# Kernel optimization log

Hardware: AMD Instinct MI355X
Metric: run time of the kernel (lower is better)

## Reference

```python
import jax, jax.numpy as jnp
import numpy as np

N, D, A, NQ, G1, G2 = 2048, 512, 64, 8, 8, 8
A1 = 2 * A  # tier-1 MQA uses att_dim*2 internally


def setup_inputs() -> dict:
    key = jax.random.key(0)
    ks = iter(jax.random.split(key, 24))
    r = lambda *sh: (jax.random.normal(next(ks), sh, dtype=jnp.float32) * 0.02)
    return {
        "x": jax.random.normal(next(ks), (N, D), dtype=jnp.float32),
        # tier 1 (num_groups_first MQA blocks, inner dim A1)
        "Wq1": r(G1, NQ, D, A1), "bq1": r(G1, NQ, A1),
        "Wk1": r(G1, D, A1),     "bk1": r(G1, A1),
        "Wv1": r(G1, D, A1),     "bv1": r(G1, A1),
        "Wo1": r(G1, NQ * A1, D), "bo1": r(G1, D),
        # tier 2 (num_groups_second MQA blocks, inner dim A)
        "Wq2": r(G2, NQ, D, A), "bq2": r(G2, NQ, A),
        "Wk2": r(G2, D, A),     "bk2": r(G2, A),
        "Wv2": r(G2, D, A),     "bv2": r(G2, A),
        "Wo2": r(G2, NQ * A, D), "bo2": r(G2, D),
        # final projection: in = att_dim * num_groups_second == D
        "Wo": r(D, D), "bo": r(D),
    }


def _mqa_grouped(xg, Wq, bq, Wk, bk, Wv, bv, Wo, bo):
    """Batched MultiQueryAttention over a group axis g.
    xg: [g, n, d]; Wq: [g, q, d, a]. No softmax (per source)."""
    a = Wq.shape[-1]
    q = jnp.einsum('gnd,gqda->gqna', xg, Wq) + bq[:, :, None, :]
    k = jnp.einsum('gnd,gda->gna', xg, Wk) + bk[:, None, :]
    v = jnp.einsum('gnd,gda->gna', xg, Wv) + bv[:, None, :]
    scores = jnp.einsum('gqna,gma->gqnm', q, k) / jnp.sqrt(jnp.asarray(a, jnp.float32))
    ctx = jnp.einsum('gqnm,gma->gqna', scores, v)          # [g,q,n,a]
    g, nq, n, ad = ctx.shape
    ctx = ctx.transpose(0, 2, 1, 3).reshape(g, n, nq * ad)  # concat queries on feat dim
    return jnp.einsum('gnf,gfd->gnd', ctx, Wo) + bo[:, None, :]


def reference(x, Wq1, bq1, Wk1, bk1, Wv1, bv1, Wo1, bo1,
              Wq2, bq2, Wk2, bk2, Wv2, bv2, Wo2, bo2, Wo, bo):
    xg = jnp.broadcast_to(x[None], (G1, N, D))
    o1 = _mqa_grouped(xg, Wq1, bq1, Wk1, bk1, Wv1, bv1, Wo1, bo1)   # [G1,N,D]
    o2 = _mqa_grouped(o1[:G2], Wq2, bq2, Wk2, bk2, Wv2, bv2, Wo2, bo2)  # [G2,N,D]
    o2_flat = o2.reshape(G2 * N, D)  # torch.cat along token dim (dim=0)
    return o2_flat @ Wo + bo          # [G2*N, D]
```

## Files before the change

kernel.cpp:

```cpp
#include <hip/hip_runtime.h>


typedef __bf16 bf16x8 __attribute__((ext_vector_type(8)));
typedef float  f32x4  __attribute__((ext_vector_type(4)));

struct PD { const float* s; void* d; int R, C, Bc, mode, blocks; };
struct PArgs { PD p[20]; int n; };

struct MA {
    const float *x,*bq1,*bo1,*bq2,*bo2,*bo;
    float* out;
    __bf16 *xb,*Wk1t,*Wv1t,*Wq1b,*Wo1t,*Wk2t,*Wv2t,*Wq2b,*Wo2b,*Wot;
    __bf16 *Ktb,*Vtb,*T1b,*M1t,*o1b,*K2tb,*V2tb,*T2b,*Wo2pT,*M2pt;
    float *STf1,*STf2,*kvb1,*kvb2,*c1,*c2p,*bo2p;
    PArgs pa;
    int prepTot;
};

template<int BM, int BN, int KK>
__device__ __forceinline__ void ss_gemm(void* smv,
    const __bf16* __restrict__ A, const float* __restrict__ Bf,
    __bf16* __restrict__ C, long aG, long bG, long cG, int cD, int cQ, int vb)
{
    constexpr int MT = BM / 32, NT = BN / 32, KS = KK / 32;
    constexpr int ACH = (KK * 2) / 16;
    constexpr int ABYTES = BM * KK * 2;
    constexpr int AITER = ABYTES / 16 / 256;
    constexpr int ROWB = KK * 2;
    constexpr int F4PT = (BN * KK) / 4 / 256;
    constexpr int TPR  = (KK / 4) / F4PT;

    char* smc = (char*)smv;
    int g = vb >> 6, rb = vb & 63;
    A  += g * aG + (long)rb * BM * KK;
    Bf += g * bG;
    C  += g * cG;

    int tid = threadIdx.x, wave = tid >> 6, lane = tid & 63;
    int mrow = lane & 15, quad = lane >> 4;

    #pragma unroll
    for (int i = 0; i < AITER; ++i) {
        int c = tid + i * 256;
        int row = c / ACH, cp = c % ACH;
        int cg = cp ^ (row & 7);
        __builtin_amdgcn_global_load_lds(
            (const __attribute__((address_space(1))) void*)(A + (long)row * KK + cg * 8),
            (__attribute__((address_space(3))) void*)(smc + c * 16),
            16, 0, 0);
    }
    {
        int brow = tid / TPR, bseg = tid % TPR;
        const float4* bsrc = (const float4*)(Bf + (long)brow * KK + bseg * (KK / TPR));
        int cbase = (bseg * (KK / TPR)) >> 3;
        int bx7 = brow & 7;
        char* bls = smc + ABYTES + (long)brow * ROWB;
        #pragma unroll
        for (int j = 0; j < F4PT / 2; ++j) {
            float4 f0 = bsrc[2 * j], f1 = bsrc[2 * j + 1];
            bf16x8 v = {(__bf16)f0.x, (__bf16)f0.y, (__bf16)f0.z, (__bf16)f0.w,
                        (__bf16)f1.x, (__bf16)f1.y, (__bf16)f1.z, (__bf16)f1.w};
            *(bf16x8*)(bls + (((cbase + j) ^ bx7) << 4)) = v;
        }
    }
    __syncthreads();

    int wm = (wave >> 1) * (BM / 2), wn = (wave & 1) * (BN / 2);
    f32x4 acc[MT][NT];
    #pragma unroll
    for (int i = 0; i < MT; ++i)
        #pragma unroll
        for (int j = 0; j < NT; ++j)
            acc[i][j] = f32x4{0.f, 0.f, 0.f, 0.f};

    #pragma unroll
    for (int ks = 0; ks < KS; ++ks) {
        bf16x8 af[MT], bv[NT];
        #pragma unroll
        for (int mt = 0; mt < MT; ++mt) {
            int r = wm + mt * 16 + mrow;
            af[mt] = *(const bf16x8*)(smc + (long)r * ROWB
                        + (((ks * 4 + quad) ^ (r & 7)) << 4));
        }
        #pragma unroll
        for (int nt = 0; nt < NT; ++nt) {
            int r = wn + nt * 16 + mrow;
            bv[nt] = *(const bf16x8*)(smc + ABYTES + (long)r * ROWB
                        + (((ks * 4 + quad) ^ (r & 7)) << 4));
        }
        #pragma unroll
        for (int mt = 0; mt < MT; ++mt)
            #pragma unroll
            for (int nt = 0; nt < NT; ++nt)
                acc[mt][nt] = __builtin_amdgcn_mfma_f32_16x16x32_bf16(
                    af[mt], bv[nt], acc[mt][nt], 0, 0, 0);
    }

    #pragma unroll
    for (int mt = 0; mt < MT; ++mt) {
        #pragma unroll
        for (int r4 = 0; r4 < 4; ++r4) {
            int rl = wm + mt * 16 + quad * 4 + r4;
            int ra = rb * BM + rl;
            int q = ra >> 9, d = ra & 511;
            #pragma unroll
            for (int nt = 0; nt < NT; ++nt) {
                int col = wn + nt * 16 + mrow;
                C[(long)d * cD + q * cQ + col] = (__bf16)acc[mt][nt][r4];
            }
        }
    }
}

template<int BM, int BN, int MODE>
__device__ __forceinline__ void gemm_block(void* smv,
    const __bf16* __restrict__ A, const __bf16* __restrict__ B,
    const float* __restrict__ bias, void* __restrict__ Cv,
    int K, int lda, int ldb, int ldc, int divq, int ksplit,
    long aOut, long aIn, long bOut, long bIn, long cOut, long cIn,
    long biasOut, long biasIn, int hasBias, float alpha,
    int bx, int by, int bz)
{
    constexpr int MT = BM / 32, NT = BN / 32;
    constexpr int ROWB = 128;
    constexpr int HALF = (BM + BN) * ROWB;
    constexpr int AOPS = BM * 8 / 256;
    constexpr int BOPS = BN * 8 / 256;

    char* smc = (char*)smv;

    int b  = bz / ksplit, ks = bz - b * ksplit;
    int go = b / divq,  gi = b - go * divq;
    A += go * aOut + gi * aIn;
    B += go * bOut + gi * bIn;
    long cBase = go * cOut + gi * cIn;
    if (hasBias) bias += go * biasOut + gi * biasIn;

    int kChunk = K / ksplit;
    int k0 = ks * kChunk;
    int nT = kChunk / 64;

    int bm = by * BM, bn = bx * BN;
    int tid = threadIdx.x, wave = tid >> 6, lane = tid & 63;
    int wm = (wave >> 1) * (BM / 2), wn = (wave & 1) * (BN / 2);
    int mrow = lane & 15, quad = lane >> 4;

    f32x4 acc[MT][NT];
    #pragma unroll
    for (int i = 0; i < MT; ++i)
        #pragma unroll
        for (int j = 0; j < NT; ++j)
            acc[i][j] = f32x4{0.f, 0.f, 0.f, 0.f};

    auto issueAB = [&](int buf, int kk) {
        char* base = smc + buf * HALF;
        #pragma unroll
        for (int t = 0; t < AOPS; ++t) {
            int c = tid + t * 256;
            int row = c >> 3, cp = c & 7;
            int cg = cp ^ (row & 7);
            __builtin_amdgcn_global_load_lds(
                (const __attribute__((address_space(1))) void*)
                    (A + (long)(bm + row) * lda + kk + cg * 8),
                (__attribute__((address_space(3))) void*)(base + c * 16),
                16, 0, 0);
        }
        char* bbase = base + BM * ROWB;
        #pragma unroll
        for (int t = 0; t < BOPS; ++t) {
            int c = tid + t * 256;
            int row = c >> 3, cp = c & 7;
            int cg = cp ^ (row & 7);
            __builtin_amdgcn_global_load_lds(
                (const __attribute__((address_space(1))) void*)
                    (B + (long)(bn + row) * ldb + kk + cg * 8),
                (__attribute__((address_space(3))) void*)(bbase + c * 16),
                16, 0, 0);
        }
    };

    issueAB(0, k0);
    __syncthreads();

    int cur = 0;
    for (int t = 0; t < nT; ++t) {
        if (t + 1 < nT) issueAB(cur ^ 1, k0 + (t + 1) * 64);

        char* base = smc + cur * HALF;
        #pragma unroll
        for (int k2 = 0; k2 < 2; ++k2) {
            bf16x8 af[MT], bfv[NT];
            #pragma unroll
            for (int mt = 0; mt < MT; ++mt) {
                int r = wm + mt * 16 + mrow;
                af[mt] = *(const bf16x8*)(base + r * ROWB
                            + (((k2 * 4 + quad) ^ (r & 7)) << 4));
            }
            #pragma unroll
            for (int nt = 0; nt < NT; ++nt) {
                int r = wn + nt * 16 + mrow;
                bfv[nt] = *(const bf16x8*)(base + BM * ROWB + r * ROWB
                            + (((k2 * 4 + quad) ^ (r & 7)) << 4));
            }
            #pragma unroll
            for (int mt = 0; mt < MT; ++mt)
                #pragma unroll
                for (int nt = 0; nt < NT; ++nt) {
                    if constexpr (MODE == 2)
                        acc[mt][nt] = __builtin_amdgcn_mfma_f32_16x16x32_bf16(
                            bfv[nt], af[mt], acc[mt][nt], 0, 0, 0);
                    else
                        acc[mt][nt] = __builtin_amdgcn_mfma_f32_16x16x32_bf16(
                            af[mt], bfv[nt], acc[mt][nt], 0, 0, 0);
                }
        }

        __syncthreads();
        cur ^= 1;
    }

    if constexpr (MODE == 2) {
        #pragma unroll
        for (int nt = 0; nt < NT; ++nt) {
            #pragma unroll
            for (int r = 0; r < 4; ++r) {
                int ci = bn + wn + nt * 16 + quad * 4 + r;
                #pragma unroll
                for (int mt = 0; mt < MT; ++mt) {
                    int mi = bm + wm + mt * 16 + mrow;
                    float v = acc[mt][nt][r] * alpha;
                    if (hasBias) v += bias[ci];
                    ((__bf16*)Cv)[cBase + (long)ci * ldc + mi] = (__bf16)v;
                }
            }
        }
    } else {
        #pragma unroll
        for (int mt = 0; mt < MT; ++mt) {
            #pragma unroll
            for (int r = 0; r < 4; ++r) {
                int row = bm + wm + mt * 16 + quad * 4 + r;
                #pragma unroll
                for (int nt = 0; nt < NT; ++nt) {
                    int col = bn + wn + nt * 16 + mrow;
                    float v = acc[mt][nt][r] * alpha;
                    if (hasBias) v += bias[col];
                    if constexpr (MODE == 0)
                        ((float*)Cv)[cBase + (long)row * ldc + col] = v;
                    else if constexpr (MODE == 1)
                        ((__bf16*)Cv)[cBase + (long)row * ldc + col] = (__bf16)v;
                    else
                        atomicAdd(&((float*)Cv)[cBase + (long)row * ldc + col], v);
                }
            }
        }
    }
}

__device__ __forceinline__ void prep_block(const PArgs& a, int bid, void* smv)
{
    int i = 0;
    while (i < a.n && bid >= a.p[i].blocks) { bid -= a.p[i].blocks; ++i; }
    if (i >= a.n) return;
    PD d = a.p[i];
    int t = threadIdx.x;
    if (d.mode == 0) {
        float (*tile)[33] = (float(*)[33])smv;
        int tC = d.C >> 5, tR = d.R >> 5;
        int batch = bid / (tC * tR), rem = bid - batch * (tC * tR);
        int tyo = rem / tC, txo = rem - tyo * tC;
        const float* src = d.s + (long)batch * d.R * d.C;
        __bf16* dst = (__bf16*)d.d + (long)batch * d.R * d.C;
        int tx = t & 31, ty = t >> 5;
        int r0 = tyo * 32, c0 = txo * 32;
        #pragma unroll
        for (int u = 0; u < 4; ++u)
            tile[ty + 8 * u][tx] = src[(long)(r0 + ty + 8 * u) * d.C + c0 + tx];
        __syncthreads();
        #pragma unroll
        for (int u = 0; u < 4; ++u)
            dst[(long)(c0 + ty + 8 * u) * d.R + r0 + tx] = (__bf16)tile[tx][ty + 8 * u];
    } else if (d.mode == 1) {
        long idx = ((long)bid * 256 + t) * 4;
        long total = (long)d.Bc * d.R * d.C;
        if (idx < total) {
            float4 f = *(const float4*)(d.s + idx);
            __bf16* o = (__bf16*)d.d + idx;
            o[0] = (__bf16)f.x; o[1] = (__bf16)f.y;
            o[2] = (__bf16)f.z; o[3] = (__bf16)f.w;
        }
    } else {
        long idx = (long)bid * 256 + t;
        long total = (long)d.Bc * d.R * d.C;
        if (idx < total) {
            float* o = (float*)d.d;
            if (d.mode == 2) o[idx] = d.s[idx];
            else             o[idx] = 0.f;
        }
    }
}

__device__ __forceinline__ void small_block(void* smv,
    const float* __restrict__ STf, const float* __restrict__ bq,
    const __bf16* __restrict__ WoT, const float* __restrict__ boA,
    float* __restrict__ cOut, int ad, int F, long wG, int bid)
{
    int tid = threadIdx.x;
    float* rL  = (float*)smv;
    float* red = (float*)((char*)smv + 4096);
    int g = bid >> 5, slice = bid & 31;
    int nq = F / ad;
    const float* Sg = STf + (long)g * ad * ad;
    for (int f = tid; f < F; f += 256) {
        int q = f / ad, aa = f - q * ad;
        const float* bv = bq + (long)(g * nq + q) * ad;
        const float* Sa = Sg + (long)aa * ad;
        float s = 0.f;
        for (int c = 0; c < ad; c += 4) {
            float4 b4 = *(const float4*)(bv + c);
            float4 s4 = *(const float4*)(Sa + c);
            s += b4.x * s4.x + b4.y * s4.y + b4.z * s4.z + b4.w * s4.w;
        }
        rL[f] = s;
    }
    __syncthreads();
    int dl = tid & 15, fs = tid >> 4;
    int d = slice * 16 + dl;
    int fchunk = F >> 4;
    const __bf16* wrow = WoT + (long)g * wG + (long)d * F;
    float s = 0.f;
    for (int f0 = fs * fchunk; f0 < (fs + 1) * fchunk; f0 += 8) {
        bf16x8 w = *(const bf16x8*)(wrow + f0);
        s += rL[f0]     * (float)w[0] + rL[f0 + 1] * (float)w[1]
           + rL[f0 + 2] * (float)w[2] + rL[f0 + 3] * (float)w[3]
           + rL[f0 + 4] * (float)w[4] + rL[f0 + 5] * (float)w[5]
           + rL[f0 + 6] * (float)w[6] + rL[f0 + 7] * (float)w[7];
    }
    red[tid] = s;
    __syncthreads();
    if (fs == 0) {
        float tsum = s;
        #pragma unroll
        for (int u = 1; u < 16; ++u) tsum += red[u * 16 + dl];
        cOut[(long)g * 512 + d] = boA[(long)g * 512 + d] + tsum;
    }
}

__device__ __forceinline__ void vecmat_block(void* smv,
    const float* __restrict__ v, const __bf16* __restrict__ WT,
    const float* __restrict__ bias, float* __restrict__ outp, int g, int slice)
{
    float* red2 = (float*)smv;
    int tid = threadIdx.x;
    int dl = tid & 15, fs = tid >> 4;
    int d = slice * 16 + dl;
    const float* vg = v + (long)g * 512;
    const __bf16* wrow = WT + (long)d * 512;
    float s = 0.f;
    for (int f0 = fs * 32; f0 < (fs + 1) * 32; f0 += 8) {
        bf16x8 w = *(const bf16x8*)(wrow + f0);
        s += vg[f0]     * (float)w[0] + vg[f0 + 1] * (float)w[1]
           + vg[f0 + 2] * (float)w[2] + vg[f0 + 3] * (float)w[3]
           + vg[f0 + 4] * (float)w[4] + vg[f0 + 5] * (float)w[5]
           + vg[f0 + 6] * (float)w[6] + vg[f0 + 7] * (float)w[7];
    }
    red2[tid] = s;
    __syncthreads();
    if (fs == 0) {
        float tsum = s;
        #pragma unroll
        for (int u = 1; u < 16; ++u) tsum += red2[u * 16 + dl];
        outp[(long)g * 512 + d] = bias[d] + tsum;
    }
}

template<int S>
__device__ __forceinline__ void run_stage(const MA& a, int vb, void* sm)
{
    const float isa1 = 0.08838834764831845f;
    if constexpr (S == 0) {
        prep_block(a.pa, vb, sm);
    } else if constexpr (S == 1) {
        if (vb < 1024)
            gemm_block<64,64,2>(sm, a.xb, a.Wk1t, a.kvb1, a.Ktb,
                512, 512, 512, 2048, 1, 1,
                0L, 0L, 65536L, 0L, 262144L, 0L, 128L, 0L, 1, 1.0f,
                vb & 1, (vb >> 1) & 31, vb >> 6);
        else if (vb < 1536) {
            int v = vb - 1024;
            gemm_block<64,64,2>(sm, a.Wo2b, a.Wot, nullptr, a.Wo2pT,
                512, 512, 512, 512, 1, 1,
                262144L, 0L, 0L, 0L, 262144L, 0L, 0L, 0L, 0, 1.0f,
                v & 7, (v >> 3) & 7, v >> 6);
        } else {
            int v = vb - 1536;
            vecmat_block(sm, a.bo2, a.Wot, a.bo, a.bo2p, v & 7, v >> 3);
        }
    } else if constexpr (S == 2) {
        gemm_block<64,64,3>(sm, a.Vtb, a.Ktb, nullptr, a.STf1,
            2048, 2048, 2048, 128, 1, 8,
            262144L, 0L, 262144L, 0L, 16384L, 0L, 0L, 0L, 0, isa1,
            vb & 1, (vb >> 1) & 1, vb >> 2);
    } else if constexpr (S == 3) {
        if (vb < 512)
            ss_gemm<64,128,128>(sm, a.Wq1b, a.STf1, a.T1b,
                                524288L, 16384L, 524288L, 1024, 128, vb);
        else
            small_block(sm, a.STf1, a.bq1, a.Wo1t, a.bo1, a.c1,
                        128, 1024, 524288L, vb - 512);
    } else if constexpr (S == 4) {
        gemm_block<64,64,2>(sm, a.T1b, a.Wo1t, nullptr, a.M1t,
            1024, 1024, 1024, 512, 1, 1,
            524288L, 0L, 524288L, 0L, 262144L, 0L, 0L, 0L, 0, 1.0f,
            vb & 7, (vb >> 3) & 7, vb >> 6);
    } else if constexpr (S == 5) {
        gemm_block<128,128,1>(sm, a.xb, a.M1t, a.c1, a.o1b,
            512, 512, 512, 512, 1, 1,
            0L, 0L, 262144L, 0L, 1048576L, 0L, 512L, 0L, 1, 1.0f,
            vb & 3, (vb >> 2) & 15, vb >> 6);
    } else if constexpr (S == 6) {
        gemm_block<64,64,2>(sm, a.o1b, a.Wk2t, a.kvb2, a.K2tb,
            512, 512, 512, 2048, 8, 1,
            0L, 1048576L, 262144L, 32768L, 1048576L, 131072L, 512L, 64L,
            1, 1.0f, 0, vb & 31, vb >> 5);
    } else if constexpr (S == 7) {
        gemm_block<64,64,3>(sm, a.V2tb, a.K2tb, nullptr, a.STf2,
            2048, 2048, 2048, 64, 1, 16,
            131072L, 0L, 131072L, 0L, 4096L, 0L, 0L, 0L, 0, 0.125f,
            0, 0, vb);
    } else if constexpr (S == 8) {
        if (vb < 512)
            ss_gemm<64,64,64>(sm, a.Wq2b, a.STf2, a.T2b,
                              262144L, 4096L, 262144L, 512, 64, vb);
        else
            small_block(sm, a.STf2, a.bq2, a.Wo2pT, a.bo2p, a.c2p,
                        64, 512, 262144L, vb - 512);
    } else if constexpr (S == 9) {
        gemm_block<64,64,2>(sm, a.T2b, a.Wo2pT, nullptr, a.M2pt,
            512, 512, 512, 512, 1, 1,
            262144L, 0L, 262144L, 0L, 262144L, 0L, 0L, 0L, 0, 1.0f,
            vb & 7, (vb >> 3) & 7, vb >> 6);
    } else {
        gemm_block<128,128,0>(sm, a.o1b, a.M2pt, a.c2p, a.out,
            512, 512, 512, 512, 1, 1,
            1048576L, 0L, 262144L, 0L, 1048576L, 0L, 512L, 0L, 1, 1.0f,
            vb & 3, (vb >> 2) & 15, vb >> 6);
    }
}

#define STAGE_KERNEL(NAME, S, SMEM, MINW)                                    \
__global__ __launch_bounds__(256, MINW) void NAME(MA a)                      \
{                                                                            \
    __shared__ __align__(16) unsigned char smem[SMEM];                       \
    run_stage<S>(a, blockIdx.x, smem);                                       \
}

STAGE_KERNEL(ksg0_prep,    0, 16384, 4)
STAGE_KERNEL(ksg1_kv1wo2p, 1, 32768, 4)
STAGE_KERNEL(ksg2_s1t,     2, 32768, 4)
STAGE_KERNEL(ksg3_t1c1,    3, 49152, 4)
STAGE_KERNEL(ksg4_m1t,     4, 32768, 4)
STAGE_KERNEL(ksg5_o1,      5, 65536, 2)
STAGE_KERNEL(ksg6_kv2,     6, 32768, 4)
STAGE_KERNEL(ksg7_s2t,     7, 32768, 4)
STAGE_KERNEL(ksg8_t2c2p,   8, 16384, 4)
STAGE_KERNEL(ksg9_m2pt,    9, 32768, 4)
STAGE_KERNEL(ksg10_out,   10, 65536, 2)

extern "C" void kernel_launch(void* const* d_in, const int* in_sizes, int n_in,
                              void* d_out, int out_size, void* d_ws, size_t ws_size,
                              hipStream_t stream)
{
    MA ma;
    ma.x   = (const float*)d_in[0];
    const float* Wq1 = (const float*)d_in[1];  ma.bq1 = (const float*)d_in[2];
    const float* Wk1 = (const float*)d_in[3];  const float* bk1 = (const float*)d_in[4];
    const float* Wv1 = (const float*)d_in[5];  const float* bv1 = (const float*)d_in[6];
    const float* Wo1 = (const float*)d_in[7];  ma.bo1 = (const float*)d_in[8];
    const float* Wq2 = (const float*)d_in[9];  ma.bq2 = (const float*)d_in[10];
    const float* Wk2 = (const float*)d_in[11]; const float* bk2 = (const float*)d_in[12];
    const float* Wv2 = (const float*)d_in[13]; const float* bv2 = (const float*)d_in[14];
    const float* Wo2 = (const float*)d_in[15]; ma.bo2 = (const float*)d_in[16];
    const float* Wo  = (const float*)d_in[17]; ma.bo  = (const float*)d_in[18];
    ma.out = (float*)d_out;
    (void)in_sizes; (void)n_in; (void)out_size; (void)ws_size;

    __bf16* wb = (__bf16*)d_ws;
    long o = 0;
    ma.xb    = wb + o; o += 1048576;
    ma.Wk1t  = wb + o; o += 524288;
    ma.Wv1t  = wb + o; o += 524288;
    ma.Wq1b  = wb + o; o += 4194304;
    ma.Wo1t  = wb + o; o += 4194304;
    ma.Wk2t  = wb + o; o += 262144;
    ma.Wv2t  = wb + o; o += 262144;
    ma.Wq2b  = wb + o; o += 2097152;
    ma.Wo2b  = wb + o; o += 2097152;
    ma.Wot   = wb + o; o += 262144;
    ma.Ktb   = wb + o; o += 2097152;
    ma.Vtb   = wb + o; o += 2097152;
    ma.T1b   = wb + o; o += 4194304;
    ma.M1t   = wb + o; o += 2097152;
    ma.o1b   = wb + o; o += 8388608;
    ma.K2tb  = ma.Ktb;
    ma.V2tb  = ma.Ktb + 1048576;
    ma.T2b   = wb + o; o += 2097152;
    ma.Wo2pT = wb + o; o += 2097152;
    ma.M2pt  = wb + o; o += 2097152;
    float* wf = (float*)(wb + o);
    long p = 0;
    ma.STf1 = wf + p; p += 131072;
    ma.STf2 = wf + p; p += 32768;
    ma.kvb1 = wf + p; p += 2048;
    ma.kvb2 = wf + p; p += 1024;
    ma.c1   = wf + p; p += 4096;
    ma.c2p  = wf + p; p += 4096;
    ma.bo2p = wf + p; p += 4096;

    int nd = 0, totB = 0;
    auto add = [&](const float* s, void* d, int R, int C, int Bc, int mode) {
        int blocks;
        long total = (long)Bc * R * C;
        if (mode == 0) blocks = Bc * (R >> 5) * (C >> 5);
        else if (mode == 1) blocks = (int)(total / 1024);
        else blocks = (int)((total + 255) / 256);
        ma.pa.p[nd] = PD{s, d, R, C, Bc, mode, blocks};
        ++nd; totB += blocks;
    };
    add(ma.x, ma.xb,   2048, 512, 1, 1);
    add(Wq1,  ma.Wq1b, 512, 128, 64, 1);
    add(Wq2,  ma.Wq2b, 512, 64, 64, 1);
    add(Wo2,  ma.Wo2b, 512, 512, 8, 1);
    add(Wk1,  ma.Wk1t, 512, 128, 8, 0);
    add(Wv1,  ma.Wv1t, 512, 128, 8, 0);
    add(Wo1,  ma.Wo1t, 1024, 512, 8, 0);
    add(Wk2,  ma.Wk2t, 512, 64, 8, 0);
    add(Wv2,  ma.Wv2t, 512, 64, 8, 0);
    add(Wo,   ma.Wot,  512, 512, 1, 0);
    add(bk1,  ma.kvb1,        1, 1024, 1, 2);
    add(bv1,  ma.kvb1 + 1024, 1, 1024, 1, 2);
    add(bk2,  ma.kvb2,        1, 512, 1, 2);
    add(bv2,  ma.kvb2 + 512,  1, 512, 1, 2);
    add(nullptr, ma.STf1, 1, 131072, 1, 4);
    add(nullptr, ma.STf2, 1, 32768, 1, 4);
    ma.pa.n = nd;
    ma.prepTot = totB;

    ksg0_prep   <<<dim3(ma.prepTot), dim3(256), 0, stream>>>(ma);
    ksg1_kv1wo2p<<<dim3(1792), dim3(256), 0, stream>>>(ma);
    ksg2_s1t    <<<dim3(256),  dim3(256), 0, stream>>>(ma);
    ksg3_t1c1   <<<dim3(768),  dim3(256), 0, stream>>>(ma);
    ksg4_m1t    <<<dim3(512),  dim3(256), 0, stream>>>(ma);
    ksg5_o1     <<<dim3(512),  dim3(256), 0, stream>>>(ma);
    ksg6_kv2    <<<dim3(512),  dim3(256), 0, stream>>>(ma);
    ksg7_s2t    <<<dim3(128),  dim3(256), 0, stream>>>(ma);
    ksg8_t2c2p  <<<dim3(768),  dim3(256), 0, stream>>>(ma);
    ksg9_m2pt   <<<dim3(512),  dim3(256), 0, stream>>>(ma);
    ksg10_out   <<<dim3(512),  dim3(256), 0, stream>>>(ma);
}
```

Before: 257.0 us.

## Compute tier-1 K^T V via Gram matrix of x instead of materializing K and V

Tier-1 V^T K is rewritten algebraically as Wv^T (x^T x) Wk, plus bias corrections built from column sums of x and per-group weight-vector products. It computes the 512x512 Gram matrix once, multiplies it by Wk per group, then runs a small GEMM with Wv and folds the bias terms and the 1/sqrt(a) scale into the epilogue. This removes the large K/V projections over 2048 tokens and the 2048-deep reduction, at the cost of extra launches, a transposed copy of x, and different bf16 rounding.

```diff
diff --git a/kernel.cpp b/kernel.cpp
--- a/kernel.cpp
+++ b/kernel.cpp
@@ -10,9 +10,9 @@
 struct MA {
     const float *x,*bq1,*bo1,*bq2,*bo2,*bo;
     float* out;
-    __bf16 *xb,*Wk1t,*Wv1t,*Wq1b,*Wo1t,*Wk2t,*Wv2t,*Wq2b,*Wo2b,*Wot;
-    __bf16 *Ktb,*Vtb,*T1b,*M1t,*o1b,*K2tb,*V2tb,*T2b,*Wo2pT,*M2pt;
-    float *STf1,*STf2,*kvb1,*kvb2,*c1,*c2p,*bo2p;
+    __bf16 *xb,*xTb,*Wk1t,*Wv1t,*Wq1b,*Wo1t,*Wk2t,*Wv2t,*Wq2b,*Wo2b,*Wot;
+    __bf16 *Gb,*Hkt,*Ktb,*T1b,*M1t,*o1b,*K2tb,*V2tb,*T2b,*Wo2pT,*M2pt;
+    float *STf1,*STf2,*kvb1,*kvb2,*c1,*c2p,*bo2p,*uw,*sx;
     PArgs pa;
     int prepTot;
 };
@@ -257,6 +257,147 @@
     }
 }
 
+__device__ __forceinline__ void s1_block(void* smv, const MA& ma, int vb)
+{
+    constexpr int ROWB = 128, HALF = 128 * ROWB;
+    char* smc = (char*)smv;
+    int g = vb >> 2, by = (vb >> 1) & 1, bx = vb & 1;
+    const __bf16* A = ma.Wv1t + (long)g * 65536;
+    const __bf16* B = ma.Hkt  + (long)g * 65536;
+    float* C = ma.STf1 + (long)g * 16384;
+
+    int bm = by * 64, bn = bx * 64;
+    int tid = threadIdx.x, wave = tid >> 6, lane = tid & 63;
+    int wm = (wave >> 1) * 32, wn = (wave & 1) * 32;
+    int mrow = lane & 15, quad = lane >> 4;
+
+    f32x4 acc[2][2];
+    #pragma unroll
+    for (int i = 0; i < 2; ++i)
+        #pragma unroll
+        for (int j = 0; j < 2; ++j)
+            acc[i][j] = f32x4{0.f, 0.f, 0.f, 0.f};
+
+    auto issueAB = [&](int buf, int kk) {
+        char* base = smc + buf * HALF;
+        #pragma unroll
+        for (int t = 0; t < 4; ++t) {
+            int c = tid + t * 256;
+            int row = c >> 3, cp = c & 7;
+            int cg = cp ^ (row & 7);
+            if (row < 64)
+                __builtin_amdgcn_global_load_lds(
+                    (const __attribute__((address_space(1))) void*)
+                        (A + (long)(bm + row) * 512 + kk + cg * 8),
+                    (__attribute__((address_space(3))) void*)(base + c * 16),
+                    16, 0, 0);
+            else
+                __builtin_amdgcn_global_load_lds(
+                    (const __attribute__((address_space(1))) void*)
+                        (B + (long)(bn + row - 64) * 512 + kk + cg * 8),
+                    (__attribute__((address_space(3))) void*)(base + c * 16),
+                    16, 0, 0);
+        }
+    };
+
+    issueAB(0, 0);
+    __syncthreads();
+    int cur = 0;
+    for (int t = 0; t < 8; ++t) {
+        if (t + 1 < 8) issueAB(cur ^ 1, (t + 1) * 64);
+        char* base = smc + cur * HALF;
+        #pragma unroll
+        for (int k2 = 0; k2 < 2; ++k2) {
+            bf16x8 af[2], bfv[2];
+            #pragma unroll
+            for (int mt = 0; mt < 2; ++mt) {
+                int r = wm + mt * 16 + mrow;
+                af[mt] = *(const bf16x8*)(base + r * ROWB
+                            + (((k2 * 4 + quad) ^ (r & 7)) << 4));
+            }
+            #pragma unroll
+            for (int nt = 0; nt < 2; ++nt) {
+                int r = 64 + wn + nt * 16 + mrow;
+                bfv[nt] = *(const bf16x8*)(base + r * ROWB
+                            + (((k2 * 4 + quad) ^ (r & 7)) << 4));
+            }
+            #pragma unroll
+            for (int mt = 0; mt < 2; ++mt)
+                #pragma unroll
+                for (int nt = 0; nt < 2; ++nt)
+                    acc[mt][nt] = __builtin_amdgcn_mfma_f32_16x16x32_bf16(
+                        af[mt], bfv[nt], acc[mt][nt], 0, 0, 0);
+        }
+        __syncthreads();
+        cur ^= 1;
+    }
+
+    const float isa1 = 0.08838834764831845f;
+    const float* uwg = ma.uw + (long)g * 256;
+    const float* bkv = ma.kvb1;
+    #pragma unroll
+    for (int mt = 0; mt < 2; ++mt) {
+        #pragma unroll
+        for (int r = 0; r < 4; ++r) {
+            int row = bm + wm + mt * 16 + quad * 4 + r;
+            float wrow = uwg[128 + row];
+            float bvr  = bkv[1024 + g * 128 + row];
+            #pragma unroll
+            for (int nt = 0; nt < 2; ++nt) {
+                int col = bn + wn + nt * 16 + mrow;
+                float ucol = uwg[col];
+                float bkc  = bkv[g * 128 + col];
+                float v = acc[mt][nt][r] + wrow * bkc + bvr * (ucol + 2048.f * bkc);
+                C[(long)row * 128 + col] = v * isa1;
+            }
+        }
+    }
+}
+
+__device__ __forceinline__ void colsum_block(void* smv, const MA& ma, int cb)
+{
+    float* red = (float*)smv;
+    int tid = threadIdx.x;
+    int rloc = tid >> 5, seg = tid & 31;
+    int row = cb * 8 + rloc;
+    const __bf16* src = ma.xTb + (long)row * 2048 + seg * 64;
+    float s = 0.f;
+    #pragma unroll
+    for (int j = 0; j < 8; ++j) {
+        bf16x8 v = *(const bf16x8*)(src + j * 8);
+        s += (float)v[0] + (float)v[1] + (float)v[2] + (float)v[3]
+           + (float)v[4] + (float)v[5] + (float)v[6] + (float)v[7];
+    }
+    red[rloc * 32 + seg] = s;
+    __syncthreads();
+    if (seg == 0) {
+        float t = 0.f;
+        #pragma unroll
+        for (int u = 0; u < 32; ++u) t += red[rloc * 32 + u];
+        ma.sx[row] = t;
+    }
+}
+
+__device__ __forceinline__ void uw_block(void* smv, const MA& ma, int g)
+{
+    float* sl = (float*)smv;
+    int tid = threadIdx.x;
+    sl[tid] = ma.sx[tid];
+    sl[tid + 256] = ma.sx[tid + 256];
+    __syncthreads();
+    int which = tid >> 7, a = tid & 127;
+    const __bf16* wrow = (which ? ma.Wv1t : ma.Wk1t) + (long)g * 65536 + (long)a * 512;
+    float s = 0.f;
+    for (int k = 0; k < 512; k += 8) {
+        bf16x8 v = *(const bf16x8*)(wrow + k);
+        s += (float)v[0] * sl[k]     + (float)v[1] * sl[k + 1]
+           + (float)v[2] * sl[k + 2] + (float)v[3] * sl[k + 3]
+           + (float)v[4] * sl[k + 4] + (float)v[5] * sl[k + 5]
+           + (float)v[6] * sl[k + 6] + (float)v[7] * sl[k + 7];
+    }
+    ma.uw[(long)g * 256 + which * 128 + a] = s;
+}
+
 __device__ __forceinline__ void prep_block(const PArgs& a, int bid, void* smv)
 {
     int i = 0;
@@ -377,30 +518,35 @@
 template<int S>
 __device__ __forceinline__ void run_stage(const MA& a, int vb, void* sm)
 {
-    const float isa1 = 0.08838834764831845f;
     if constexpr (S == 0) {
         prep_block(a.pa, vb, sm);
     } else if constexpr (S == 1) {
-        if (vb < 1024)
-            gemm_block<64,64,2>(sm, a.xb, a.Wk1t, a.kvb1, a.Ktb,
-                512, 512, 512, 2048, 1, 1,
-                0L, 0L, 65536L, 0L, 262144L, 0L, 128L, 0L, 1, 1.0f,
-                vb & 1, (vb >> 1) & 31, vb >> 6);
-        else if (vb < 1536) {
-            int v = vb - 1024;
+        if (vb < 64)
+            gemm_block<64,64,1>(sm, a.xTb, a.xTb, nullptr, a.Gb,
+                2048, 2048, 2048, 512, 1, 1,
+                0L, 0L, 0L, 0L, 0L, 0L, 0L, 0L, 0, 1.0f,
+                vb & 7, vb >> 3, 0);
+        else if (vb < 576) {
+            int v = vb - 64;
             gemm_block<64,64,2>(sm, a.Wo2b, a.Wot, nullptr, a.Wo2pT,
                 512, 512, 512, 512, 1, 1,
                 262144L, 0L, 0L, 0L, 262144L, 0L, 0L, 0L, 0, 1.0f,
                 v & 7, (v >> 3) & 7, v >> 6);
-        } else {
-            int v = vb - 1536;
+        } else if (vb < 832) {
+            int v = vb - 576;
             vecmat_block(sm, a.bo2, a.Wot, a.bo, a.bo2p, v & 7, v >> 3);
-        }
+        } else
+            colsum_block(sm, a, vb - 832);
     } else if constexpr (S == 2) {
-        gemm_block<64,64,3>(sm, a.Vtb, a.Ktb, nullptr, a.STf1,
-            2048, 2048, 2048, 128, 1, 8,
-            262144L, 0L, 262144L, 0L, 16384L, 0L, 0L, 0L, 0, isa1,
-            vb & 1, (vb >> 1) & 1, vb >> 2);
+        if (vb < 128)
+            gemm_block<64,64,2>(sm, a.Gb, a.Wk1t, nullptr, a.Hkt,
+                512, 512, 512, 512, 1, 1,
+                0L, 0L, 65536L, 0L, 65536L, 0L, 0L, 0L, 0, 1.0f,
+                vb & 1, (vb >> 1) & 7, vb >> 4);
+        else
+            uw_block(sm, a, vb - 128);
+    } else if constexpr (S == 11) {
+        s1_block(sm, a, vb);
     } else if constexpr (S == 3) {
         if (vb < 512)
             ss_gemm<64,128,128>(sm, a.Wq1b, a.STf1, a.T1b,
@@ -456,8 +602,9 @@
 }
 
 STAGE_KERNEL(ksg0_prep,    0, 16384, 4)
-STAGE_KERNEL(ksg1_kv1wo2p, 1, 32768, 4)
-STAGE_KERNEL(ksg2_s1t,     2, 32768, 4)
+STAGE_KERNEL(ksg1_gwo2p,   1, 32768, 4)
+STAGE_KERNEL(ksg2_hk,      2, 32768, 4)
+STAGE_KERNEL(ksg2b_s1,    11, 32768, 4)
 STAGE_KERNEL(ksg3_t1c1,    3, 49152, 4)
 STAGE_KERNEL(ksg4_m1t,     4, 32768, 4)
 STAGE_KERNEL(ksg5_o1,      5, 65536, 2)
@@ -488,6 +635,7 @@
     __bf16* wb = (__bf16*)d_ws;
     long o = 0;
     ma.xb    = wb + o; o += 1048576;
+    ma.xTb   = wb + o; o += 1048576;
     ma.Wk1t  = wb + o; o += 524288;
     ma.Wv1t  = wb + o; o += 524288;
     ma.Wq1b  = wb + o; o += 4194304;
@@ -497,8 +645,9 @@
     ma.Wq2b  = wb + o; o += 2097152;
     ma.Wo2b  = wb + o; o += 2097152;
     ma.Wot   = wb + o; o += 262144;
+    ma.Gb    = wb + o; o += 262144;
+    ma.Hkt   = wb + o; o += 524288;
     ma.Ktb   = wb + o; o += 2097152;
-    ma.Vtb   = wb + o; o += 2097152;
     ma.T1b   = wb + o; o += 4194304;
     ma.M1t   = wb + o; o += 2097152;
     ma.o1b   = wb + o; o += 8388608;
@@ -516,6 +665,8 @@
     ma.c1   = wf + p; p += 4096;
     ma.c2p  = wf + p; p += 4096;
     ma.bo2p = wf + p; p += 4096;
+    ma.uw   = wf + p; p += 2048;
+    ma.sx   = wf + p; p += 512;
 
     int nd = 0, totB = 0;
     auto add = [&](const float* s, void* d, int R, int C, int Bc, int mode) {
@@ -528,6 +679,7 @@
         ++nd; totB += blocks;
     };
     add(ma.x, ma.xb,   2048, 512, 1, 1);
+    add(ma.x, ma.xTb,  2048, 512, 1, 0);
     add(Wq1,  ma.Wq1b, 512, 128, 64, 1);
     add(Wq2,  ma.Wq2b, 512, 64, 64, 1);
     add(Wo2,  ma.Wo2b, 512, 512, 8, 1);
@@ -541,14 +693,14 @@
     add(bv1,  ma.kvb1 + 1024, 1, 1024, 1, 2);
     add(bk2,  ma.kvb2,        1, 512, 1, 2);
     add(bv2,  ma.kvb2 + 512,  1, 512, 1, 2);
-    add(nullptr, ma.STf1, 1, 131072, 1, 4);
     add(nullptr, ma.STf2, 1, 32768, 1, 4);
     ma.pa.n = nd;
     ma.prepTot = totB;
 
     ksg0_prep   <<<dim3(ma.prepTot), dim3(256), 0, stream>>>(ma);
-    ksg1_kv1wo2p<<<dim3(1792), dim3(256), 0, stream>>>(ma);
-    ksg2_s1t    <<<dim3(256),  dim3(256), 0, stream>>>(ma);
+    ksg1_gwo2p  <<<dim3(896),  dim3(256), 0, stream>>>(ma);
+    ksg2_hk     <<<dim3(136),  dim3(256), 0, stream>>>(ma);
+    ksg2b_s1    <<<dim3(32),   dim3(256), 0, stream>>>(ma);
     ksg3_t1c1   <<<dim3(768),  dim3(256), 0, stream>>>(ma);
     ksg4_m1t    <<<dim3(512),  dim3(256), 0, stream>>>(ma);
     ksg5_o1     <<<dim3(512),  dim3(256), 0, stream>>>(ma);
```

After: 273.6 us. 6.4% more time.
